# Optimization experiments

Measured on AMD Instinct MI355X. Metric: run time of the kernel, lower is better.

## Reference

```python
import jax, jax.numpy as jnp
import numpy as np

EPS = 1e-5  # torch LayerNorm default
NUM_HEADS = 12


def layer_norm(x, g, b):
    m = jnp.mean(x, axis=-1, keepdims=True)
    v = jnp.var(x, axis=-1, keepdims=True)
    return (x - m) * jax.lax.rsqrt(v + EPS) * g + b


def split_heads(x):
    B, N, C = x.shape
    return x.reshape(B, N, NUM_HEADS, C // NUM_HEADS).transpose(0, 2, 1, 3)  # [B,H,N,D]


def merge_heads(x):
    B, H, N, D = x.shape
    return x.transpose(0, 2, 1, 3).reshape(B, N, H * D)


def attn_core(q, k, v, mask):
    # q:[B,H,Nq,D], k/v:[B,H,Nk,D], mask:[B,Nk] float (1=keep)
    d = q.shape[-1]
    scores = jnp.einsum('bhqd,bhkd->bhqk', q, k) * (d ** -0.5)
    scores = scores + (1.0 - mask)[:, None, None, :] * -5.0
    a = jax.nn.softmax(scores, axis=-1)
    return jnp.einsum('bhqk,bhkd->bhqd', a, v)


def setup_inputs() -> dict:
    key = jax.random.key(0)
    B, N, C = 4, 1024, 768
    Hd = C * 4  # mlp hidden = 3072
    ks = jax.random.split(key, 12)
    s = 0.02
    inp = {
        'x': jax.random.normal(ks[0], (B, N, C), jnp.float32),
        'encoder_out': jax.random.normal(ks[1], (B, N, C), jnp.float32),
        'mask': jnp.ones((B, N), jnp.float32),
        'encoder_mask': jnp.ones((B, N), jnp.float32),
        'ln1_g': jnp.ones((C,), jnp.float32), 'ln1_b': jnp.zeros((C,), jnp.float32),
        'qkv_w': jax.random.normal(ks[2], (C, 3 * C), jnp.float32) * s,
        'sa_proj_w': jax.random.normal(ks[3], (C, C), jnp.float32) * s,
        'sa_proj_b': jnp.zeros((C,), jnp.float32),
        'ln2_g': jnp.ones((C,), jnp.float32), 'ln2_b': jnp.zeros((C,), jnp.float32),
        'q_w': jax.random.normal(ks[4], (C, C), jnp.float32) * s,
        'kv_w': jax.random.normal(ks[5], (C, 2 * C), jnp.float32) * s,
        'ca_proj_w': jax.random.normal(ks[6], (C, C), jnp.float32) * s,
        'ca_proj_b': jnp.zeros((C,), jnp.float32),
        'ln3_g': jnp.ones((C,), jnp.float32), 'ln3_b': jnp.zeros((C,), jnp.float32),
        'fc1_w': jax.random.normal(ks[7], (C, Hd), jnp.float32) * s,
        'fc1_b': jnp.zeros((Hd,), jnp.float32),
        'fc2_w': jax.random.normal(ks[8], (Hd, C), jnp.float32) * s,
        'fc2_b': jnp.zeros((C,), jnp.float32),
    }
    return inp


def reference(x, encoder_out, mask, encoder_mask,
              ln1_g, ln1_b, qkv_w, sa_proj_w, sa_proj_b,
              ln2_g, ln2_b, q_w, kv_w, ca_proj_w, ca_proj_b,
              ln3_g, ln3_b, fc1_w, fc1_b, fc2_w, fc2_b):
    B, N, C = x.shape
    D = C // NUM_HEADS
    # --- self attention ---
    h = layer_norm(x, ln1_g, ln1_b)
    qkv = (h @ qkv_w).reshape(B, N, 3, NUM_HEADS, D)
    q = qkv[:, :, 0].transpose(0, 2, 1, 3)
    k = qkv[:, :, 1].transpose(0, 2, 1, 3)
    v = qkv[:, :, 2].transpose(0, 2, 1, 3)
    o = merge_heads(attn_core(q, k, v, mask)) @ sa_proj_w + sa_proj_b
    x = x + o
    # --- cross attention ---
    h = layer_norm(x, ln2_g, ln2_b)
    q = split_heads(h @ q_w)
    Be, Ne, Ce = encoder_out.shape
    kv = (encoder_out @ kv_w).reshape(Be, Ne, 2, NUM_HEADS, D)
    k = kv[:, :, 0].transpose(0, 2, 1, 3)
    v = kv[:, :, 1].transpose(0, 2, 1, 3)
    o = merge_heads(attn_core(q, k, v, encoder_mask)) @ ca_proj_w + ca_proj_b
    x = x + o
    # --- MLP (exact GELU, like torch nn.GELU default) ---
    h = layer_norm(x, ln3_g, ln3_b)
    h = jax.nn.gelu(h @ fc1_w + fc1_b, approximate=False) @ fc2_w + fc2_b
    return x + h
```

## Files before the change

kernel.cpp:

```cpp
#include <hip/hip_runtime.h>

typedef __attribute__((ext_vector_type(8))) __bf16 bf16x8;
typedef __attribute__((ext_vector_type(4))) float f32x4;

__device__ __forceinline__ void gload_lds16(const __bf16* g, __bf16* l) {
    __builtin_amdgcn_global_load_lds(
        (const __attribute__((address_space(1))) void*)g,
        (__attribute__((address_space(3))) void*)l,
        16, 0, 0);
}

template <int N> struct WaitVm;
#define WV(n) template <> struct WaitVm<n> { static __device__ __forceinline__ void run() { \
    asm volatile("s_waitcnt vmcnt(" #n ")" ::: "memory"); } };
WV(0) WV(3) WV(4) WV(6) WV(8) WV(9) WV(12)
#undef WV

__device__ __forceinline__ float gelu_f(float x) {
    float z = fabsf(x) * 0.70710678118f;
    float t = 1.0f / (1.0f + 0.3275911f * z);
    float poly = t * (0.254829592f + t * (-0.284496736f +
                 t * (1.421413741f + t * (-1.453152027f + t * 1.061405429f))));
    float erfv = 1.0f - poly * __expf(-z * z);
    erfv = (x < 0.f) ? -erfv : erfv;
    return 0.5f * x * (1.0f + erfv);
}

__global__ __launch_bounds__(256) void prep_all(
    const float* __restrict__ qkv_w, __bf16* __restrict__ qkv_t,
    const float* __restrict__ sa_w,  __bf16* __restrict__ sa_t,
    const float* __restrict__ q_w,   __bf16* __restrict__ q_t,
    const float* __restrict__ kv_w,  __bf16* __restrict__ kv_t,
    const float* __restrict__ ca_w,  __bf16* __restrict__ ca_t,
    const float* __restrict__ fc1_w, __bf16* __restrict__ fc1_t,
    const float* __restrict__ fc2_w, __bf16* __restrict__ fc2_t,
    const float* __restrict__ enc,   __bf16* __restrict__ encb) {
    __shared__ __bf16 tile[32][33];
    const int b = blockIdx.x;
    const float* in; __bf16* out; int R, C, l;
    if (b < 1728)      { in = qkv_w; out = qkv_t; R = 768;  C = 2304; l = b; }
    else if (b < 2304) { in = sa_w;  out = sa_t;  R = 768;  C = 768;  l = b - 1728; }
    else if (b < 2880) { in = q_w;   out = q_t;   R = 768;  C = 768;  l = b - 2304; }
    else if (b < 4032) { in = kv_w;  out = kv_t;  R = 768;  C = 1536; l = b - 2880; }
    else if (b < 4608) { in = ca_w;  out = ca_t;  R = 768;  C = 768;  l = b - 4032; }
    else if (b < 6912) { in = fc1_w; out = fc1_t; R = 768;  C = 3072; l = b - 4608; }
    else if (b < 9216) { in = fc2_w; out = fc2_t; R = 3072; C = 768;  l = b - 6912; }
    else {
        int i = (b - 9216) * 256 + threadIdx.x;
        float4 v = ((const float4*)enc)[i];
        __bf16 o4[4] = {(__bf16)v.x, (__bf16)v.y, (__bf16)v.z, (__bf16)v.w};
        *(uint2*)(encb + (size_t)i * 4) = *(const uint2*)o4;
        return;
    }
    const int txn = C >> 5;
    const int bx = (l % txn) << 5, by = (l / txn) << 5;
    const int tx = threadIdx.x & 31, ty = threadIdx.x >> 5;
#pragma unroll
    for (int i = ty; i < 32; i += 8)
        tile[i][tx] = (__bf16)in[(size_t)(by + i) * C + bx + tx];
    __syncthreads();
#pragma unroll
    for (int i = ty; i < 32; i += 8)
        out[(size_t)(bx + i) * R + by + tx] = tile[tx][i];
}

__global__ __launch_bounds__(256) void ln_kernel(const float* __restrict__ x,
                                                 const float* __restrict__ g,
                                                 const float* __restrict__ b,
                                                 __bf16* __restrict__ o) {
    int row = blockIdx.x, tid = threadIdx.x;
    const float* xr = x + (size_t)row * 768;
    float v0 = xr[tid], v1 = xr[tid + 256], v2 = xr[tid + 512];
    float s = v0 + v1 + v2, s2 = v0 * v0 + v1 * v1 + v2 * v2;
#pragma unroll
    for (int d = 32; d >= 1; d >>= 1) {
        s += __shfl_xor(s, d);
        s2 += __shfl_xor(s2, d);
    }
    __shared__ float red[8];
    int wave = tid >> 6, lane = tid & 63;
    if (!lane) { red[wave] = s; red[4 + wave] = s2; }
    __syncthreads();
    s = red[0] + red[1] + red[2] + red[3];
    s2 = red[4] + red[5] + red[6] + red[7];
    float mean = s * (1.0f / 768.0f);
    float var = s2 * (1.0f / 768.0f) - mean * mean;
    float inv = rsqrtf(var + 1e-5f);
    o[(size_t)row * 768 + tid]       = (__bf16)((v0 - mean) * inv * g[tid]       + b[tid]);
    o[(size_t)row * 768 + tid + 256] = (__bf16)((v1 - mean) * inv * g[tid + 256] + b[tid + 256]);
    o[(size_t)row * 768 + tid + 512] = (__bf16)((v2 - mean) * inv * g[tid + 512] + b[tid + 512]);
}

template <int BIAS, int RESID, int GELU, typename TO>
__global__ __launch_bounds__(256) void reduce_splitk(
    const float* __restrict__ P, TO* __restrict__ C,
    const float* __restrict__ bias, const float* __restrict__ resid,
    int total4, int ncols) {
    int i = blockIdx.x * 256 + threadIdx.x;
    if (i >= total4) return;
    float4 a = ((const float4*)P)[i];
    float4 b = ((const float4*)P)[i + total4];
    float v[4] = {a.x + b.x, a.y + b.y, a.z + b.z, a.w + b.w};
    int col = (i * 4) % ncols;
    if (BIAS) {
        float4 bs = *(const float4*)(bias + col);
        v[0] += bs.x; v[1] += bs.y; v[2] += bs.z; v[3] += bs.w;
    }
    if (GELU)
#pragma unroll
        for (int j = 0; j < 4; ++j) v[j] = gelu_f(v[j]);
    if (RESID) {
        float4 r = ((const float4*)resid)[i];
        v[0] += r.x; v[1] += r.y; v[2] += r.z; v[3] += r.w;
    }
    ((TO*)C)[(size_t)i * 4]     = (TO)v[0];
    ((TO*)C)[(size_t)i * 4 + 1] = (TO)v[1];
    ((TO*)C)[(size_t)i * 4 + 2] = (TO)v[2];
    ((TO*)C)[(size_t)i * 4 + 3] = (TO)v[3];
}

template <int BM, int NS, int SPLITK, int BIAS, int RESID, int GELU, int SWZ, typename TO>
__global__ __launch_bounds__(256, 2) void gemm_nt(
    const __bf16* __restrict__ A, int lda,
    const __bf16* __restrict__ Bt, int ldb,
    TO* __restrict__ C, int ldc,
    const float* __restrict__ bias,
    const float* __restrict__ resid,
    int K) {
    __shared__ __bf16 lA[NS][BM * 32];
    __shared__ __bf16 lB[NS][128 * 32];
    constexpr int L = (BM == 128) ? 4 : 3;
    constexpr int WCOLS = 256 / BM;
    constexpr int NF = (BM == 128) ? 4 : 2;
    constexpr int WNSP = (BM == 128) ? 64 : 32;
    const int tid = threadIdx.x;
    const int wave = tid >> 6, lane = tid & 63;
    const int wm = wave / WCOLS, wn = wave % WCOLS;
    const int ln15 = lane & 15, hi = lane >> 4;

    int bn, bm;
    if constexpr (SWZ) {
        const int lin = blockIdx.x + blockIdx.y * gridDim.x;
        const int nwg = gridDim.x * gridDim.y;
        const int t0 = (lin & 7) * (nwg >> 3) + (lin >> 3);
        bn = (t0 % gridDim.x) * 128; bm = (t0 / gridDim.x) * BM;
    } else {
        bn = blockIdx.x * 128; bm = blockIdx.y * BM;
    }

    if constexpr (SPLITK > 1) {
        const int kz = blockIdx.z;
        K /= SPLITK;
        A += (size_t)kz * K;
        Bt += (size_t)kz * K;
        C += (size_t)kz * 4096 * ldc;
    }

    f32x4 acc[4][NF] = {};

    const int srow = tid >> 2;
    const int scol = (((tid & 3) ^ ((srow >> 1) & 3)) * 8);
    const __bf16* gA0 = A + (size_t)(bm + srow) * lda + scol;
    const __bf16* gA1 = A + (size_t)(bm + 64 + srow) * lda + scol;
    const __bf16* gB0 = Bt + (size_t)(bn + srow) * ldb + scol;
    const __bf16* gB1 = Bt + (size_t)(bn + 64 + srow) * ldb + scol;

    const int rswz = (hi * 8) ^ (((ln15 >> 1) & 3) * 8);
    const int rAoff = (wm * 64 + ln15) * 32 + rswz;
    const int rBoff = (wn * WNSP + ln15) * 32 + rswz;

    auto STAGE = [&](int buf, int k0) {
        gload_lds16(gA0 + k0, lA[buf] + wave * 512);
        if constexpr (BM == 128) gload_lds16(gA1 + k0, lA[buf] + 2048 + wave * 512);
        gload_lds16(gB0 + k0, lB[buf] + wave * 512);
        gload_lds16(gB1 + k0, lB[buf] + 2048 + wave * 512);
    };
    auto COMPUTE = [&](int buf) {
        const __bf16* rA = lA[buf] + rAoff;
        const __bf16* rB = lB[buf] + rBoff;
        bf16x8 af[4], bfr[NF];
#pragma unroll
        for (int m = 0; m < 4; ++m) af[m] = *(const bf16x8*)(rA + m * 512);
#pragma unroll
        for (int n = 0; n < NF; ++n) bfr[n] = *(const bf16x8*)(rB + n * 512);
#pragma unroll
        for (int m = 0; m < 4; ++m)
#pragma unroll
            for (int n = 0; n < NF; ++n)
                acc[m][n] = __builtin_amdgcn_mfma_f32_16x16x32_bf16(af[m], bfr[n], acc[m][n], 0, 0, 0);
    };
    auto inc = [](int b) { return (b + 1 == NS) ? 0 : b + 1; };

    const int nt = K >> 5;
#pragma unroll
    for (int s = 0; s < NS - 1; ++s) STAGE(s, s << 5);
    int sbuf = NS - 1, cbuf = 0;
    for (int t = 0; t <= nt - NS; ++t) {
        STAGE(sbuf, (t + NS - 1) << 5);
        sbuf = inc(sbuf);
        WaitVm<(NS - 1) * L>::run();
        __builtin_amdgcn_s_barrier();
        __builtin_amdgcn_sched_barrier(0);
        COMPUTE(cbuf);
        cbuf = inc(cbuf);
        __builtin_amdgcn_sched_barrier(0);
        __builtin_amdgcn_s_barrier();
    }
    if constexpr (NS >= 4) {
        WaitVm<2 * L>::run();
        __builtin_amdgcn_s_barrier();
        __builtin_amdgcn_sched_barrier(0);
        COMPUTE(cbuf); cbuf = inc(cbuf);
        __builtin_amdgcn_sched_barrier(0);
        __builtin_amdgcn_s_barrier();
    }
    if constexpr (NS >= 3) {
        WaitVm<L>::run();
        __builtin_amdgcn_s_barrier();
        __builtin_amdgcn_sched_barrier(0);
        COMPUTE(cbuf); cbuf = inc(cbuf);
        __builtin_amdgcn_sched_barrier(0);
        __builtin_amdgcn_s_barrier();
    }
    WaitVm<0>::run();
    __builtin_amdgcn_s_barrier();
    __builtin_amdgcn_sched_barrier(0);
    COMPUTE(cbuf);

#pragma unroll
    for (int m = 0; m < 4; ++m)
#pragma unroll
        for (int n = 0; n < NF; ++n)
#pragma unroll
            for (int r = 0; r < 4; ++r) {
                int row = bm + wm * 64 + m * 16 + hi * 4 + r;
                int col = bn + wn * WNSP + n * 16 + ln15;
                float v = acc[m][n][r];
                if (BIAS) v += bias[col];
                if (GELU) v = gelu_f(v);
                if (RESID) v += resid[(size_t)row * ldc + col];
                C[(size_t)row * ldc + col] = (TO)v;
            }
}

__global__ __launch_bounds__(256, 2) void attn_kernel(
    const __bf16* __restrict__ Qp, int ldq, int qcol,
    const __bf16* __restrict__ Kp, int ldk, int kcol,
    const __bf16* __restrict__ Vp, int ldv, int vcol,
    const float* __restrict__ mask,
    __bf16* __restrict__ Out) {
    __shared__ __bf16 lK[64 * 64];
    __shared__ __bf16 lV[64 * 64];
    __shared__ __bf16 lP[4][16 * 64];
    const int tid = threadIdx.x, wave = tid >> 6, lane = tid & 63;
    const int lin = blockIdx.x + blockIdx.y * 16;
    const int t0 = (lin & 7) * 96 + (lin >> 3);
    const int qt = t0 & 15, bh = t0 >> 4;
    const int b = bh / 12, h = bh % 12;
    const int ln15 = lane & 15, hi = lane >> 4;

    const __bf16* qrow = Qp + (size_t)(b * 1024 + qt * 64 + wave * 16 + ln15) * ldq + qcol + h * 64;
    bf16x8 qf0 = *(const bf16x8*)(qrow + hi * 8);
    bf16x8 qf1 = *(const bf16x8*)(qrow + 32 + hi * 8);

    float l_part[4] = {0.f, 0.f, 0.f, 0.f};
    f32x4 oacc[4] = {};

    const int skey = tid >> 3;
    const int ssrc = (((tid & 7) ^ (skey & 7)) * 8);
    const __bf16* gK = Kp + (size_t)(b * 1024 + skey) * ldk + kcol + h * 64 + ssrc;
    __bf16* lK0 = lK + wave * 512;
    __bf16* lK1 = lK + 2048 + wave * 512;

    const int vkey = tid & 63;
    const int vdb = wave * 16;
    const __bf16* gV = Vp + (size_t)(b * 1024 + vkey) * ldv + vcol + h * 64 + vdb;

    const int kswz = (lane & 7) * 8;
    const __bf16* rK = lK + ln15 * 64;
    const __bf16* rV = lV + ln15 * 64;
    __bf16* wP = lP[wave];
    const __bf16* rP = lP[wave] + ln15 * 64;

    const float C1 = 0.18033688f;
    for (int kt = 0; kt < 16; ++kt) {
        const size_t tb = (size_t)kt * 64;
        gload_lds16(gK + tb * ldk, lK0);
        gload_lds16(gK + (tb + 32) * ldk, lK1);
        bf16x8 v0 = *(const bf16x8*)(gV + tb * ldv);
        bf16x8 v1 = *(const bf16x8*)(gV + tb * ldv + 8);
#pragma unroll
        for (int j = 0; j < 8; ++j) {
            lV[(vdb + j) * 64 + (vkey ^ (j * 8))] = v0[j];
            lV[(vdb + 8 + j) * 64 + (vkey ^ (j * 8))] = v1[j];
        }
        __syncthreads();

        f32x4 s[4];
#pragma unroll
        for (int n = 0; n < 4; ++n) {
            bf16x8 kf0 = *(const bf16x8*)(rK + n * 1024 + ((hi * 8) ^ kswz));
            bf16x8 kf1 = *(const bf16x8*)(rK + n * 1024 + ((hi * 8 + 32) ^ kswz));
            f32x4 z = {};
            z = __builtin_amdgcn_mfma_f32_16x16x32_bf16(qf0, kf0, z, 0, 0, 0);
            s[n] = __builtin_amdgcn_mfma_f32_16x16x32_bf16(qf1, kf1, z, 0, 0, 0);
        }
        float mb2[4];
#pragma unroll
        for (int n = 0; n < 4; ++n)
            mb2[n] = (1.0f - mask[b * 1024 + kt * 64 + n * 16 + ln15]) * -7.2134752f;

#pragma unroll
        for (int n = 0; n < 4; ++n)
#pragma unroll
            for (int r = 0; r < 4; ++r) {
                s[n][r] = exp2f(s[n][r] * C1 + mb2[n]);
                l_part[r] += s[n][r];
            }

#pragma unroll
        for (int n = 0; n < 4; ++n)
#pragma unroll
            for (int r = 0; r < 4; ++r) {
                int prow = hi * 4 + r;
                wP[prow * 64 + ((n * 16 + ln15) ^ ((prow & 7) * 8))] = (__bf16)s[n][r];
            }
        bf16x8 pf0 = *(const bf16x8*)(rP + ((hi * 8) ^ kswz));
        bf16x8 pf1 = *(const bf16x8*)(rP + ((hi * 8 + 32) ^ kswz));
#pragma unroll
        for (int n = 0; n < 4; ++n) {
            bf16x8 vf0 = *(const bf16x8*)(rV + n * 1024 + ((hi * 8) ^ kswz));
            bf16x8 vf1 = *(const bf16x8*)(rV + n * 1024 + ((hi * 8 + 32) ^ kswz));
            oacc[n] = __builtin_amdgcn_mfma_f32_16x16x32_bf16(pf0, vf0, oacc[n], 0, 0, 0);
            oacc[n] = __builtin_amdgcn_mfma_f32_16x16x32_bf16(pf1, vf1, oacc[n], 0, 0, 0);
        }
        __syncthreads();
    }

#pragma unroll
    for (int r = 0; r < 4; ++r) {
#pragma unroll
        for (int d = 1; d < 16; d <<= 1) l_part[r] += __shfl_xor(l_part[r], d);
        l_part[r] = 1.0f / l_part[r];
    }

#pragma unroll
    for (int n = 0; n < 4; ++n)
#pragma unroll
        for (int r = 0; r < 4; ++r) {
            int row = b * 1024 + qt * 64 + wave * 16 + hi * 4 + r;
            int col = h * 64 + n * 16 + ln15;
            Out[(size_t)row * 768 + col] = (__bf16)(oacc[n][r] * l_part[r]);
        }
}

extern "C" void kernel_launch(void* const* d_in, const int* in_sizes, int n_in,
                              void* d_out, int out_size, void* d_ws, size_t ws_size,
                              hipStream_t stream) {
    const float* x     = (const float*)d_in[0];
    const float* enc   = (const float*)d_in[1];
    const float* mask  = (const float*)d_in[2];
    const float* emask = (const float*)d_in[3];
    const float* ln1_g = (const float*)d_in[4];
    const float* ln1_b = (const float*)d_in[5];
    const float* qkv_w = (const float*)d_in[6];
    const float* sa_w  = (const float*)d_in[7];
    const float* sa_b  = (const float*)d_in[8];
    const float* ln2_g = (const float*)d_in[9];
    const float* ln2_b = (const float*)d_in[10];
    const float* q_w   = (const float*)d_in[11];
    const float* kv_w  = (const float*)d_in[12];
    const float* ca_w  = (const float*)d_in[13];
    const float* ca_b  = (const float*)d_in[14];
    const float* ln3_g = (const float*)d_in[15];
    const float* ln3_b = (const float*)d_in[16];
    const float* fc1_w = (const float*)d_in[17];
    const float* fc1_b = (const float*)d_in[18];
    const float* fc2_w = (const float*)d_in[19];
    const float* fc2_b = (const float*)d_in[20];
    float* out = (float*)d_out;

    char* w = (char*)d_ws;
    size_t off = 0;
    auto alloc = [&](size_t bytes) { void* p = w + off; off += bytes; return p; };
    __bf16* qkv_t = (__bf16*)alloc((size_t)2304 * 768 * 2);
    __bf16* sa_t  = (__bf16*)alloc((size_t)768 * 768 * 2);
    __bf16* q_t   = (__bf16*)alloc((size_t)768 * 768 * 2);
    __bf16* kv_t  = (__bf16*)alloc((size_t)1536 * 768 * 2);
    __bf16* ca_t  = (__bf16*)alloc((size_t)768 * 768 * 2);
    __bf16* fc1_t = (__bf16*)alloc((size_t)3072 * 768 * 2);
    __bf16* fc2_t = (__bf16*)alloc((size_t)768 * 3072 * 2);
    __bf16* H     = (__bf16*)alloc((size_t)4096 * 768 * 2);
    __bf16* QKV   = (__bf16*)alloc((size_t)4096 * 2304 * 2);
    __bf16* ATT   = (__bf16*)alloc((size_t)4096 * 768 * 2);
    float*  X1    = (float*)alloc((size_t)4096 * 768 * 4);
    float*  X2    = (float*)alloc((size_t)4096 * 768 * 4);
    __bf16* encb  = (__bf16*)alloc((size_t)4096 * 768 * 2);
    float*  PK    = (float*)alloc((size_t)2 * 4096 * 768 * 4);
    __bf16* HID   = QKV;
    __bf16* Qb    = QKV;
    __bf16* KVb   = QKV + (size_t)4096 * 768;

    dim3 blk(256);
    prep_all<<<dim3(12288), blk, 0, stream>>>(qkv_w, qkv_t, sa_w, sa_t, q_w, q_t,
                                              kv_w, kv_t, ca_w, ca_t, fc1_w, fc1_t,
                                              fc2_w, fc2_t, enc, encb);

    ln_kernel<<<4096, blk, 0, stream>>>(x, ln1_g, ln1_b, H);
    gemm_nt<128, 3, 1, 0, 0, 0, 1, __bf16><<<dim3(18, 32), blk, 0, stream>>>(H, 768, qkv_t, 768, QKV, 2304, nullptr, nullptr, 768);
    attn_kernel<<<dim3(16, 48), blk, 0, stream>>>(QKV, 2304, 0, QKV, 2304, 768, QKV, 2304, 1536, mask, ATT);
    gemm_nt<64, 4, 1, 1, 1, 0, 1, float><<<dim3(6, 64), blk, 0, stream>>>(ATT, 768, sa_t, 768, X1, 768, sa_b, x, 768);
    ln_kernel<<<4096, blk, 0, stream>>>(X1, ln2_g, ln2_b, H);
    gemm_nt<64, 4, 1, 0, 0, 0, 1, __bf16><<<dim3(6, 64), blk, 0, stream>>>(H, 768, q_t, 768, Qb, 768, nullptr, nullptr, 768);
    gemm_nt<128, 3, 1, 0, 0, 0, 1, __bf16><<<dim3(12, 32), blk, 0, stream>>>(encb, 768, kv_t, 768, KVb, 1536, nullptr, nullptr, 768);
    attn_kernel<<<dim3(16, 48), blk, 0, stream>>>(Qb, 768, 0, KVb, 1536, 0, KVb, 1536, 768, emask, ATT);
    gemm_nt<64, 4, 1, 1, 1, 0, 1, float><<<dim3(6, 64), blk, 0, stream>>>(ATT, 768, ca_t, 768, X2, 768, ca_b, X1, 768);
    ln_kernel<<<4096, blk, 0, stream>>>(X2, ln3_g, ln3_b, H);
    gemm_nt<64, 2, 1, 1, 0, 1, 0, __bf16><<<dim3(24, 64), blk, 0, stream>>>(H, 768, fc1_t, 768, HID, 3072, fc1_b, nullptr, 768);
    gemm_nt<64, 4, 2, 0, 0, 0, 1, float><<<dim3(6, 64, 2), blk, 0, stream>>>(HID, 3072, fc2_t, 3072, PK, 768, nullptr, nullptr, 3072);
    reduce_splitk<1, 1, 0, float><<<dim3(3072), blk, 0, stream>>>(PK, out, fc2_b, X2, 786432, 768);
}
```

Measured before the change: 405.1 us.

## Use one-barrier ring pipeline in GEMM with prefetch depth below stage count

Adds a prefetch-depth template parameter D to the GEMM and rewrites the main loop so each iteration uses a single barrier, dropping the trailing barrier. Correctness relies on keeping D ≤ NS-2 so a slack buffer is never overwritten while another wave still reads it. The cost is a shallower prefetch: for example, the QKV GEMM goes from prefetch depth 2 to 1. The fc1 GEMM grows from 2 to 3 stages to allow this, which raises its LDS use.

```diff
diff --git a/kernel.cpp b/kernel.cpp
--- a/kernel.cpp
+++ b/kernel.cpp
@@ -119,7 +119,7 @@
     ((TO*)C)[(size_t)i * 4 + 3] = (TO)v[3];
 }
 
-template <int BM, int NS, int SPLITK, int BIAS, int RESID, int GELU, int SWZ, typename TO>
+template <int BM, int NS, int D, int SPLITK, int BIAS, int RESID, int GELU, int SWZ, typename TO>
 __global__ __launch_bounds__(256, 2) void gemm_nt(
     const __bf16* __restrict__ A, int lda,
     const __bf16* __restrict__ Bt, int ldb,
@@ -133,6 +133,7 @@
     constexpr int WCOLS = 256 / BM;
     constexpr int NF = (BM == 128) ? 4 : 2;
     constexpr int WNSP = (BM == 128) ? 64 : 32;
+    static_assert(D <= NS - 2, "one-barrier ring needs D <= NS-2");
     const int tid = threadIdx.x;
     const int wave = tid >> 6, lane = tid & 63;
     const int wm = wave / WCOLS, wn = wave % WCOLS;
@@ -193,34 +194,24 @@
 
     const int nt = K >> 5;
 #pragma unroll
-    for (int s = 0; s < NS - 1; ++s) STAGE(s, s << 5);
-    int sbuf = NS - 1, cbuf = 0;
-    for (int t = 0; t <= nt - NS; ++t) {
-        STAGE(sbuf, (t + NS - 1) << 5);
+    for (int s = 0; s < D; ++s) STAGE(s, s << 5);
+    int sbuf = D % NS, cbuf = 0;
+    for (int t = 0; t < nt - D; ++t) {
+        STAGE(sbuf, (t + D) << 5);
         sbuf = inc(sbuf);
-        WaitVm<(NS - 1) * L>::run();
+        WaitVm<D * L>::run();
         __builtin_amdgcn_s_barrier();
         __builtin_amdgcn_sched_barrier(0);
         COMPUTE(cbuf);
         cbuf = inc(cbuf);
         __builtin_amdgcn_sched_barrier(0);
-        __builtin_amdgcn_s_barrier();
-    }
-    if constexpr (NS >= 4) {
-        WaitVm<2 * L>::run();
-        __builtin_amdgcn_s_barrier();
-        __builtin_amdgcn_sched_barrier(0);
-        COMPUTE(cbuf); cbuf = inc(cbuf);
-        __builtin_amdgcn_sched_barrier(0);
-        __builtin_amdgcn_s_barrier();
-    }
-    if constexpr (NS >= 3) {
+    }
+    if constexpr (D >= 2) {
         WaitVm<L>::run();
         __builtin_amdgcn_s_barrier();
         __builtin_amdgcn_sched_barrier(0);
         COMPUTE(cbuf); cbuf = inc(cbuf);
         __builtin_amdgcn_sched_barrier(0);
-        __builtin_amdgcn_s_barrier();
     }
     WaitVm<0>::run();
     __builtin_amdgcn_s_barrier();
@@ -407,16 +398,16 @@
                                               fc2_w, fc2_t, enc, encb);
 
     ln_kernel<<<4096, blk, 0, stream>>>(x, ln1_g, ln1_b, H);
-    gemm_nt<128, 3, 1, 0, 0, 0, 1, __bf16><<<dim3(18, 32), blk, 0, stream>>>(H, 768, qkv_t, 768, QKV, 2304, nullptr, nullptr, 768);
+    gemm_nt<128, 3, 1, 1, 0, 0, 0, 1, __bf16><<<dim3(18, 32), blk, 0, stream>>>(H, 768, qkv_t, 768, QKV, 2304, nullptr, nullptr, 768);
     attn_kernel<<<dim3(16, 48), blk, 0, stream>>>(QKV, 2304, 0, QKV, 2304, 768, QKV, 2304, 1536, mask, ATT);
-    gemm_nt<64, 4, 1, 1, 1, 0, 1, float><<<dim3(6, 64), blk, 0, stream>>>(ATT, 768, sa_t, 768, X1, 768, sa_b, x, 768);
+    gemm_nt<64, 4, 2, 1, 1, 1, 0, 1, float><<<dim3(6, 64), blk, 0, stream>>>(ATT, 768, sa_t, 768, X1, 768, sa_b, x, 768);
     ln_kernel<<<4096, blk, 0, stream>>>(X1, ln2_g, ln2_b, H);
-    gemm_nt<64, 4, 1, 0, 0, 0, 1, __bf16><<<dim3(6, 64), blk, 0, stream>>>(H, 768, q_t, 768, Qb, 768, nullptr, nullptr, 768);
-    gemm_nt<128, 3, 1, 0, 0, 0, 1, __bf16><<<dim3(12, 32), blk, 0, stream>>>(encb, 768, kv_t, 768, KVb, 1536, nullptr, nullptr, 768);
+    gemm_nt<64, 4, 2, 1, 0, 0, 0, 1, __bf16><<<dim3(6, 64), blk, 0, stream>>>(H, 768, q_t, 768, Qb, 768, nullptr, nullptr, 768);
+    gemm_nt<128, 3, 1, 1, 0, 0, 0, 1, __bf16><<<dim3(12, 32), blk, 0, stream>>>(encb, 768, kv_t, 768, KVb, 1536, nullptr, nullptr, 768);
     attn_kernel<<<dim3(16, 48), blk, 0, stream>>>(Qb, 768, 0, KVb, 1536, 0, KVb, 1536, 768, emask, ATT);
-    gemm_nt<64, 4, 1, 1, 1, 0, 1, float><<<dim3(6, 64), blk, 0, stream>>>(ATT, 768, ca_t, 768, X2, 768, ca_b, X1, 768);
+    gemm_nt<64, 4, 2, 1, 1, 1, 0, 1, float><<<dim3(6, 64), blk, 0, stream>>>(ATT, 768, ca_t, 768, X2, 768, ca_b, X1, 768);
     ln_kernel<<<4096, blk, 0, stream>>>(X2, ln3_g, ln3_b, H);
-    gemm_nt<64, 2, 1, 1, 0, 1, 0, __bf16><<<dim3(24, 64), blk, 0, stream>>>(H, 768, fc1_t, 768, HID, 3072, fc1_b, nullptr, 768);
-    gemm_nt<64, 4, 2, 0, 0, 0, 1, float><<<dim3(6, 64, 2), blk, 0, stream>>>(HID, 3072, fc2_t, 3072, PK, 768, nullptr, nullptr, 3072);
+    gemm_nt<64, 3, 1, 1, 1, 0, 1, 0, __bf16><<<dim3(24, 64), blk, 0, stream>>>(H, 768, fc1_t, 768, HID, 3072, fc1_b, nullptr, 768);
+    gemm_nt<64, 4, 2, 2, 0, 0, 0, 1, float><<<dim3(6, 64, 2), blk, 0, stream>>>(HID, 3072, fc2_t, 3072, PK, 768, nullptr, nullptr, 3072);
     reduce_splitk<1, 1, 0, float><<<dim3(3072), blk, 0, stream>>>(PK, out, fc2_b, X2, 786432, 768);
 }
```

After: 401.4 us. About the same (-0.9%).
